# Kernel optimization log

Hardware: AMD Instinct MI355X
Metric: run time of the kernel (lower is better)

Reference implementation:

```python
import jax, jax.numpy as jnp
import numpy as np

N_NODES = 100000
N_EDGES = 3200000
F_IN = 64
HID = 20
N_GRAPHS = 128
N_CLASSES = 10
EPS_NORM = 1e-12  # torch F.normalize eps


def setup_inputs() -> dict:
    key = jax.random.key(0)
    ks = jax.random.split(key, 16)
    x = jax.random.normal(ks[0], (N_NODES, F_IN), dtype=jnp.float32)
    edge_index = jax.random.randint(ks[1], (2, N_EDGES), 0, N_NODES, dtype=jnp.int64)
    batch = jnp.sort(jax.random.randint(ks[2], (N_NODES,), 0, N_GRAPHS, dtype=jnp.int64))
    edge_weights = jnp.ones((N_EDGES,), dtype=jnp.float32)

    def lin_init(k, fan_in, fan_out):
        kw, kb = jax.random.split(k)
        bound = 1.0 / np.sqrt(fan_in)
        W = jax.random.uniform(kw, (fan_in, fan_out), jnp.float32, -bound, bound)
        b = jax.random.uniform(kb, (fan_out,), jnp.float32, -bound, bound)
        return W, b

    W1a, b1a = lin_init(ks[3], F_IN, HID)
    W1b, b1b = lin_init(ks[4], HID, HID)
    W2a, b2a = lin_init(ks[5], HID, HID)
    W2b, b2b = lin_init(ks[6], HID, HID)
    W3a, b3a = lin_init(ks[7], HID, HID)
    W3b, b3b = lin_init(ks[8], HID, HID)
    Wlin, blin = lin_init(ks[9], 2 * HID, N_CLASSES)
    return dict(x=x, edge_index=edge_index, batch=batch, edge_weights=edge_weights,
                W1a=W1a, b1a=b1a, W1b=W1b, b1b=b1b,
                W2a=W2a, b2a=b2a, W2b=W2b, b2b=b2b,
                W3a=W3a, b3a=b3a, W3b=W3b, b3b=b3b,
                Wlin=Wlin, blin=blin)


def _gin_layer(h, src, dst, w, Wa, ba, Wb, bb):
    # scatter-add aggregation: agg[dst] += h[src] * w   (no self-loop / central term
    # because edge_weight is provided in GINConv_mask.forward)
    msg = h[src] * w[:, None]                              # [E, d]
    agg = jax.ops.segment_sum(msg, dst, num_segments=N_NODES)
    z = jax.nn.relu(agg @ Wa + ba)
    z = jax.nn.relu(z @ Wb + bb)
    # per-node L2 normalize then ReLU
    nrm = jnp.sqrt(jnp.sum(z * z, axis=1, keepdims=True))
    z = z / jnp.maximum(nrm, EPS_NORM)
    return jax.nn.relu(z)


def reference(x, edge_index, batch, edge_weights,
              W1a, b1a, W1b, b1b, W2a, b2a, W2b, b2b, W3a, b3a, W3b, b3b,
              Wlin, blin):
    src, dst = edge_index[0], edge_index[1]
    h = _gin_layer(x, src, dst, edge_weights, W1a, b1a, W1b, b1b)
    h = _gin_layer(h, src, dst, edge_weights, W2a, b2a, W2b, b2b)
    h = _gin_layer(h, src, dst, edge_weights, W3a, b3a, W3b, b3b)  # [N, 20]

    # global max / mean pool per graph
    mx = jax.ops.segment_max(h, batch, num_segments=N_GRAPHS)
    counts = jax.ops.segment_sum(jnp.ones((N_NODES,), h.dtype), batch, num_segments=N_GRAPHS)
    sm = jax.ops.segment_sum(h, batch, num_segments=N_GRAPHS)
    mean = sm / jnp.maximum(counts, 1.0)[:, None]
    mx = jnp.where(counts[:, None] > 0, mx, 0.0)
    pooled = jnp.concatenate([mx, mean], axis=-1)          # [G, 40]
    return pooled @ Wlin + blin                            # [G, num_classes]
```

## Files before the change

### kernel.cpp

```cpp
#include <hip/hip_runtime.h>
#include <hip/hip_fp16.h>
#include <math.h>

#define NN 100000
#define NE 3200000
#define FIN 64
#define HID 20
#define NG 128
#define NC 10

#define BSH 8
#define NB1 391
#define NB1P 392
#define NBLK1 1024
#define E1 (NE / NBLK1)

__global__ __launch_bounds__(256) void k_in_gemm_h(const float* __restrict__ x,
                                                   const float* __restrict__ W,
                                                   __half* __restrict__ t) {
    __shared__ float sW[FIN * HID];
    for (int i = threadIdx.x; i < FIN * HID; i += blockDim.x) sW[i] = W[i];
    __syncthreads();
    int node = blockIdx.x * blockDim.x + threadIdx.x;
    if (node >= NN) return;
    float acc[HID];
#pragma unroll
    for (int f = 0; f < HID; ++f) acc[f] = 0.f;
    const float4* xr = (const float4*)(x + node * FIN);
#pragma unroll 4
    for (int q = 0; q < FIN / 4; ++q) {
        float4 xv = xr[q];
        int k = q * 4;
#pragma unroll
        for (int f = 0; f < HID; ++f) acc[f] += xv.x * sW[(k + 0) * HID + f];
#pragma unroll
        for (int f = 0; f < HID; ++f) acc[f] += xv.y * sW[(k + 1) * HID + f];
#pragma unroll
        for (int f = 0; f < HID; ++f) acc[f] += xv.z * sW[(k + 2) * HID + f];
#pragma unroll
        for (int f = 0; f < HID; ++f) acc[f] += xv.w * sW[(k + 3) * HID + f];
    }
    uint32_t* orow = (uint32_t*)t + (size_t)node * (HID / 2);
#pragma unroll
    for (int m = 0; m < HID / 2; ++m) {
        __half2 hh = __floats2half2_rn(acc[2 * m], acc[2 * m + 1]);
        orow[m] = *reinterpret_cast<uint32_t*>(&hh);
    }
}

__global__ __launch_bounds__(256) void k_p1count(const int* __restrict__ dst,
                                                 int* __restrict__ ghist) {
    __shared__ int h[NB1];
    for (int i = threadIdx.x; i < NB1; i += 256) h[i] = 0;
    __syncthreads();
    int base = blockIdx.x * E1;
    for (int i = threadIdx.x; i < E1; i += 256)
        atomicAdd(&h[dst[base + i] >> BSH], 1);
    __syncthreads();
    for (int b = threadIdx.x; b < NB1; b += 256)
        ghist[b * NBLK1 + blockIdx.x] = h[b];
}

__global__ __launch_bounds__(256) void k_breduceB(const int* __restrict__ ghist,
                                                  int* __restrict__ bsum) {
    int bin = blockIdx.x;
    int s = 0;
    for (int i = threadIdx.x; i < NBLK1; i += 256) s += ghist[bin * NBLK1 + i];
    __shared__ int r[256];
    r[threadIdx.x] = s;
    __syncthreads();
    for (int o = 128; o > 0; o >>= 1) {
        if (threadIdx.x < o) r[threadIdx.x] += r[threadIdx.x + o];
        __syncthreads();
    }
    if (threadIdx.x == 0) bsum[bin] = r[0];
}

__global__ __launch_bounds__(256) void k_bscanB(const int* __restrict__ bsum,
                                                int* __restrict__ bstart) {
    __shared__ int s[NB1];
    for (int i = threadIdx.x; i < NB1; i += 256) s[i] = bsum[i];
    __syncthreads();
    if (threadIdx.x == 0) {
        int acc = 0;
        for (int i = 0; i < NB1; ++i) { int v = s[i]; s[i] = acc; acc += v; }
    }
    __syncthreads();
    for (int i = threadIdx.x; i < NB1; i += 256) bstart[i] = s[i];
    if (threadIdx.x == 0) bstart[NB1] = NE;
}

__global__ __launch_bounds__(256) void k_bbase(const int* __restrict__ ghist,
                                               const int* __restrict__ bstart,
                                               int* __restrict__ gbase) {
    int bin = blockIdx.x;
    int t = threadIdx.x;
    int v[4];
    int s = 0;
    int base = bin * NBLK1 + t * 4;
#pragma unroll
    for (int k = 0; k < 4; ++k) { v[k] = ghist[base + k]; s += v[k]; }
    __shared__ int tsum[256];
    tsum[t] = s;
    __syncthreads();
    for (int d = 1; d < 256; d <<= 1) {
        int add = (t >= d) ? tsum[t - d] : 0;
        __syncthreads();
        tsum[t] += add;
        __syncthreads();
    }
    int excl = tsum[t] - s + bstart[bin];
#pragma unroll
    for (int k = 0; k < 4; ++k) {
        gbase[(size_t)(t * 4 + k) * NB1P + bin] = excl;
        excl += v[k];
    }
}

__global__ __launch_bounds__(256) void k_p1scatter(const int* __restrict__ src,
                                                   const int* __restrict__ dst,
                                                   const float* __restrict__ w,
                                                   const int* __restrict__ gbase,
                                                   int2* __restrict__ part) {
    __shared__ int cur[NB1];
    int t = threadIdx.x;
    for (int b = t; b < NB1; b += 256) cur[b] = gbase[(size_t)blockIdx.x * NB1P + b];
    __syncthreads();
    int base = blockIdx.x * E1;
    for (int i = t; i < E1; i += 256) {
        int e = base + i;
        int d = dst[e];
        int b = d >> BSH;
        int pos = atomicAdd(&cur[b], 1);
        part[pos] = make_int2(src[e] | ((d & 255) << 17), __float_as_int(w[e]));
    }
}

__global__ __launch_bounds__(256) void k_p2(const int2* __restrict__ part,
                                            const int* __restrict__ bstart,
                                            int2* __restrict__ csr,
                                            int* __restrict__ off) {
    int b = blockIdx.x;
    int lo = bstart[b], hi = bstart[b + 1];
    int t = threadIdx.x;
    __shared__ int hist[256];
    hist[t] = 0;
    __syncthreads();
    for (int i = lo + t; i < hi; i += 256)
        atomicAdd(&hist[part[i].x >> 17], 1);
    __syncthreads();
    int a = hist[t];
    __shared__ int tsum[256];
    tsum[t] = a;
    __syncthreads();
    for (int d = 1; d < 256; d <<= 1) {
        int add = (t >= d) ? tsum[t - d] : 0;
        __syncthreads();
        tsum[t] += add;
        __syncthreads();
    }
    int excl = tsum[t] - a;
    __shared__ int cur[256];
    cur[t] = lo + excl;
    int node = (b << BSH) + t;
    if (node < NN) off[node] = lo + excl;
    if (b == NB1 - 1 && t == 0) off[NN] = NE;
    __syncthreads();
    for (int i = lo + t; i < hi; i += 256) {
        int2 pr = part[i];
        int ld = pr.x >> 17;
        int pos = atomicAdd(&cur[ld], 1);
        csr[pos] = make_int2(pr.x & 0x1FFFF, pr.y);
    }
}

template <bool LAST>
__global__ __launch_bounds__(256) void k_layer(const int* __restrict__ off,
                                               const int2* __restrict__ csr,
                                               const __half* __restrict__ tin,
                                               const float* __restrict__ ba,
                                               const float* __restrict__ Wb,
                                               const float* __restrict__ bb,
                                               const float* __restrict__ Wnext,
                                               __half* __restrict__ tout) {
    __shared__ float sWb[HID * HID];
    __shared__ float sWn[HID * HID];
    __shared__ float sba[HID], sbb[HID];
    for (int i = threadIdx.x; i < HID * HID; i += blockDim.x) {
        sWb[i] = Wb[i];
        if (!LAST) sWn[i] = Wnext[i];
    }
    if (threadIdx.x < HID) {
        sba[threadIdx.x] = ba[threadIdx.x];
        sbb[threadIdx.x] = bb[threadIdx.x];
    }
    __syncthreads();

    int tid = blockIdx.x * blockDim.x + threadIdx.x;
    int node = tid >> 2;
    int j = tid & 3;
    if (node >= NN) return;
    int lo = off[node], hi = off[node + 1];

    float acc[HID];
#pragma unroll
    for (int f = 0; f < HID; ++f) acc[f] = 0.f;

    for (int i = lo + j; i < hi; i += 4) {
        int2 pr = csr[i];
        float wt = __int_as_float(pr.y);
        const uint2* r = (const uint2*)tin + (size_t)pr.x * 5;
#pragma unroll
        for (int k = 0; k < 5; ++k) {
            uint2 u = r[k];
            __half2 h0 = *reinterpret_cast<const __half2*>(&u.x);
            __half2 h1 = *reinterpret_cast<const __half2*>(&u.y);
            float2 f0 = __half22float2(h0);
            float2 f1 = __half22float2(h1);
            acc[4 * k + 0] += wt * f0.x;
            acc[4 * k + 1] += wt * f0.y;
            acc[4 * k + 2] += wt * f1.x;
            acc[4 * k + 3] += wt * f1.y;
        }
    }
#pragma unroll
    for (int f = 0; f < HID; ++f) {
        acc[f] += __shfl_xor(acc[f], 1);
        acc[f] += __shfl_xor(acc[f], 2);
    }

    float z1[HID];
#pragma unroll
    for (int f = 0; f < HID; ++f) z1[f] = fmaxf(acc[f] + sba[f], 0.f);

    float z2[HID];
#pragma unroll
    for (int fo = 0; fo < HID; ++fo) {
        float a = sbb[fo];
#pragma unroll
        for (int k = 0; k < HID; ++k) a += z1[k] * sWb[k * HID + fo];
        z2[fo] = fmaxf(a, 0.f);
    }

    float ss = 0.f;
#pragma unroll
    for (int f = 0; f < HID; ++f) ss += z2[f] * z2[f];
    float scale = 1.f / fmaxf(sqrtf(ss), 1e-12f);
#pragma unroll
    for (int f = 0; f < HID; ++f) z2[f] *= scale;

    float res[HID];
    if (LAST) {
#pragma unroll
        for (int f = 0; f < HID; ++f) res[f] = z2[f];
    } else {
#pragma unroll
        for (int fo = 0; fo < HID; ++fo) {
            float a = 0.f;
#pragma unroll
            for (int k = 0; k < HID; ++k) a += z2[k] * sWn[k * HID + fo];
            res[fo] = a;
        }
    }

    uint32_t* orow = (uint32_t*)tout + (size_t)node * (HID / 2);
#pragma unroll
    for (int m0 = 0; m0 < 12; m0 += 4) {
        int m = m0 + j;
        if (m < HID / 2) {
            __half2 hh = __floats2half2_rn(res[2 * m], res[2 * m + 1]);
            orow[m] = *reinterpret_cast<uint32_t*>(&hh);
        }
    }
}

__global__ __launch_bounds__(256) void k_pool_h(const __half* __restrict__ h,
                                                const int* __restrict__ batch,
                                                const float* __restrict__ Wlin,
                                                const float* __restrict__ blin,
                                                float* __restrict__ out) {
    int g = blockIdx.x;
    __shared__ int s_lo, s_hi;
    if (threadIdx.x == 0) {
        int a = 0, b = NN;
        while (a < b) { int m = (a + b) >> 1; if (batch[m] < g) a = m + 1; else b = m; }
        s_lo = a;
        b = NN;
        while (a < b) { int m = (a + b) >> 1; if (batch[m] < g + 1) a = m + 1; else b = m; }
        s_hi = a;
    }
    __syncthreads();
    int lo = s_lo, hi = s_hi;

    float sm[HID], mx[HID];
#pragma unroll
    for (int f = 0; f < HID; ++f) { sm[f] = 0.f; mx[f] = 0.f; }

    for (int i = lo + threadIdx.x; i < hi; i += blockDim.x) {
        const uint2* hr = (const uint2*)h + (size_t)i * 5;
#pragma unroll
        for (int k = 0; k < 5; ++k) {
            uint2 u = hr[k];
            __half2 h0 = *reinterpret_cast<const __half2*>(&u.x);
            __half2 h1 = *reinterpret_cast<const __half2*>(&u.y);
            float2 f0 = __half22float2(h0);
            float2 f1 = __half22float2(h1);
            sm[4 * k + 0] += f0.x; mx[4 * k + 0] = fmaxf(mx[4 * k + 0], f0.x);
            sm[4 * k + 1] += f0.y; mx[4 * k + 1] = fmaxf(mx[4 * k + 1], f0.y);
            sm[4 * k + 2] += f1.x; mx[4 * k + 2] = fmaxf(mx[4 * k + 2], f1.x);
            sm[4 * k + 3] += f1.y; mx[4 * k + 3] = fmaxf(mx[4 * k + 3], f1.y);
        }
    }

#pragma unroll
    for (int f = 0; f < HID; ++f) {
        float s = sm[f], m = mx[f];
        for (int off = 32; off > 0; off >>= 1) {
            s += __shfl_down(s, off);
            m = fmaxf(m, __shfl_down(m, off));
        }
        sm[f] = s; mx[f] = m;
    }

    __shared__ float psum[4][HID], pmax[4][HID];
    int wave = threadIdx.x >> 6;
    int lane = threadIdx.x & 63;
    if (lane == 0) {
#pragma unroll
        for (int f = 0; f < HID; ++f) { psum[wave][f] = sm[f]; pmax[wave][f] = mx[f]; }
    }
    __syncthreads();

    __shared__ float fsum[HID], fmax_[HID];
    if (threadIdx.x < HID) {
        int f = threadIdx.x;
        fsum[f] = psum[0][f] + psum[1][f] + psum[2][f] + psum[3][f];
        fmax_[f] = fmaxf(fmaxf(pmax[0][f], pmax[1][f]), fmaxf(pmax[2][f], pmax[3][f]));
    }
    __syncthreads();

    if (threadIdx.x < NC) {
        int c = threadIdx.x;
        float cnt = (float)(hi - lo);
        float inv = 1.f / fmaxf(cnt, 1.f);
        float o = blin[c];
#pragma unroll
        for (int f = 0; f < HID; ++f) {
            o += fmax_[f] * Wlin[f * NC + c];
            o += (fsum[f] * inv) * Wlin[(HID + f) * NC + c];
        }
        out[g * NC + c] = o;
    }
}

__global__ __launch_bounds__(256) void k_in_gemm(const float* __restrict__ x,
                                                 const float* __restrict__ W,
                                                 float* __restrict__ t) {
    __shared__ float sW[FIN * HID];
    for (int i = threadIdx.x; i < FIN * HID; i += blockDim.x) sW[i] = W[i];
    __syncthreads();
    int node = blockIdx.x * blockDim.x + threadIdx.x;
    if (node >= NN) return;
    float acc[HID];
#pragma unroll
    for (int f = 0; f < HID; ++f) acc[f] = 0.f;
    const float4* xr = (const float4*)(x + node * FIN);
    for (int q = 0; q < FIN / 4; ++q) {
        float4 xv = xr[q];
        int k = q * 4;
#pragma unroll
        for (int f = 0; f < HID; ++f)
            acc[f] += xv.x * sW[k * HID + f] + xv.y * sW[(k + 1) * HID + f] +
                      xv.z * sW[(k + 2) * HID + f] + xv.w * sW[(k + 3) * HID + f];
    }
    float4* tr = (float4*)(t + node * HID);
#pragma unroll
    for (int q = 0; q < HID / 4; ++q) {
        float4 v;
        v.x = acc[q * 4 + 0]; v.y = acc[q * 4 + 1];
        v.z = acc[q * 4 + 2]; v.w = acc[q * 4 + 3];
        tr[q] = v;
    }
}

__global__ __launch_bounds__(256) void k_scatter(const int* __restrict__ src,
                                                 const int* __restrict__ dst,
                                                 const float* __restrict__ w,
                                                 const float* __restrict__ t,
                                                 float* __restrict__ agg) {
    int e = blockIdx.x * blockDim.x + threadIdx.x;
    if (e >= NE) return;
    int s = src[e];
    int d = dst[e];
    float wt = w[e];
    const float4* tr = (const float4*)(t + (long)s * HID);
    float* ar = agg + (long)d * HID;
#pragma unroll
    for (int q = 0; q < HID / 4; ++q) {
        float4 v = tr[q];
        atomicAdd(ar + q * 4 + 0, v.x * wt);
        atomicAdd(ar + q * 4 + 1, v.y * wt);
        atomicAdd(ar + q * 4 + 2, v.z * wt);
        atomicAdd(ar + q * 4 + 3, v.w * wt);
    }
}

template <bool LAST>
__global__ __launch_bounds__(256) void k_node(const float* agg,
                                              const float* __restrict__ ba,
                                              const float* __restrict__ Wb,
                                              const float* __restrict__ bb,
                                              const float* __restrict__ Wnext,
                                              float* out) {
    __shared__ float sWb[HID * HID];
    __shared__ float sWn[HID * HID];
    __shared__ float sba[HID], sbb[HID];
    for (int i = threadIdx.x; i < HID * HID; i += blockDim.x) {
        sWb[i] = Wb[i];
        if (!LAST) sWn[i] = Wnext[i];
    }
    if (threadIdx.x < HID) {
        sba[threadIdx.x] = ba[threadIdx.x];
        sbb[threadIdx.x] = bb[threadIdx.x];
    }
    __syncthreads();
    int node = blockIdx.x * blockDim.x + threadIdx.x;
    if (node >= NN) return;

    float z1[HID];
    const float4* ar = (const float4*)(agg + (long)node * HID);
#pragma unroll
    for (int q = 0; q < HID / 4; ++q) {
        float4 v = ar[q];
        z1[q * 4 + 0] = v.x; z1[q * 4 + 1] = v.y;
        z1[q * 4 + 2] = v.z; z1[q * 4 + 3] = v.w;
    }
#pragma unroll
    for (int f = 0; f < HID; ++f) z1[f] = fmaxf(z1[f] + sba[f], 0.f);

    float z2[HID];
#pragma unroll
    for (int fo = 0; fo < HID; ++fo) {
        float a = sbb[fo];
#pragma unroll
        for (int k = 0; k < HID; ++k) a += z1[k] * sWb[k * HID + fo];
        z2[fo] = fmaxf(a, 0.f);
    }
    float ss = 0.f;
#pragma unroll
    for (int f = 0; f < HID; ++f) ss += z2[f] * z2[f];
    float scale = 1.f / fmaxf(sqrtf(ss), 1e-12f);
#pragma unroll
    for (int f = 0; f < HID; ++f) z2[f] *= scale;

    float res[HID];
    if (LAST) {
#pragma unroll
        for (int f = 0; f < HID; ++f) res[f] = z2[f];
    } else {
#pragma unroll
        for (int fo = 0; fo < HID; ++fo) {
            float a = 0.f;
#pragma unroll
            for (int k = 0; k < HID; ++k) a += z2[k] * sWn[k * HID + fo];
            res[fo] = a;
        }
    }
    float4* orow = (float4*)(out + (long)node * HID);
#pragma unroll
    for (int q = 0; q < HID / 4; ++q) {
        float4 v;
        v.x = res[q * 4 + 0]; v.y = res[q * 4 + 1];
        v.z = res[q * 4 + 2]; v.w = res[q * 4 + 3];
        orow[q] = v;
    }
}

__global__ __launch_bounds__(256) void k_pool(const float* __restrict__ h,
                                              const int* __restrict__ batch,
                                              const float* __restrict__ Wlin,
                                              const float* __restrict__ blin,
                                              float* __restrict__ out) {
    int g = blockIdx.x;
    __shared__ int s_lo, s_hi;
    if (threadIdx.x == 0) {
        int a = 0, b = NN;
        while (a < b) { int m = (a + b) >> 1; if (batch[m] < g) a = m + 1; else b = m; }
        s_lo = a;
        b = NN;
        while (a < b) { int m = (a + b) >> 1; if (batch[m] < g + 1) a = m + 1; else b = m; }
        s_hi = a;
    }
    __syncthreads();
    int lo = s_lo, hi = s_hi;
    float sm[HID], mx[HID];
#pragma unroll
    for (int f = 0; f < HID; ++f) { sm[f] = 0.f; mx[f] = 0.f; }
    for (int i = lo + threadIdx.x; i < hi; i += blockDim.x) {
        const float4* hr = (const float4*)(h + (long)i * HID);
#pragma unroll
        for (int q = 0; q < HID / 4; ++q) {
            float4 v = hr[q];
            sm[q * 4 + 0] += v.x; mx[q * 4 + 0] = fmaxf(mx[q * 4 + 0], v.x);
            sm[q * 4 + 1] += v.y; mx[q * 4 + 1] = fmaxf(mx[q * 4 + 1], v.y);
            sm[q * 4 + 2] += v.z; mx[q * 4 + 2] = fmaxf(mx[q * 4 + 2], v.z);
            sm[q * 4 + 3] += v.w; mx[q * 4 + 3] = fmaxf(mx[q * 4 + 3], v.w);
        }
    }
#pragma unroll
    for (int f = 0; f < HID; ++f) {
        float s = sm[f], m = mx[f];
        for (int off = 32; off > 0; off >>= 1) {
            s += __shfl_down(s, off);
            m = fmaxf(m, __shfl_down(m, off));
        }
        sm[f] = s; mx[f] = m;
    }
    __shared__ float psum[4][HID], pmax[4][HID];
    int wave = threadIdx.x >> 6;
    int lane = threadIdx.x & 63;
    if (lane == 0) {
#pragma unroll
        for (int f = 0; f < HID; ++f) { psum[wave][f] = sm[f]; pmax[wave][f] = mx[f]; }
    }
    __syncthreads();
    __shared__ float fsum[HID], fmax_[HID];
    if (threadIdx.x < HID) {
        int f = threadIdx.x;
        fsum[f] = psum[0][f] + psum[1][f] + psum[2][f] + psum[3][f];
        fmax_[f] = fmaxf(fmaxf(pmax[0][f], pmax[1][f]), fmaxf(pmax[2][f], pmax[3][f]));
    }
    __syncthreads();
    if (threadIdx.x < NC) {
        int c = threadIdx.x;
        float cnt = (float)(hi - lo);
        float inv = 1.f / fmaxf(cnt, 1.f);
        float o = blin[c];
#pragma unroll
        for (int f = 0; f < HID; ++f) {
            o += fmax_[f] * Wlin[f * NC + c];
            o += (fsum[f] * inv) * Wlin[(HID + f) * NC + c];
        }
        out[g * NC + c] = o;
    }
}

extern "C" void kernel_launch(void* const* d_in, const int* in_sizes, int n_in,
                              void* d_out, int out_size, void* d_ws, size_t ws_size,
                              hipStream_t stream) {
    const float* x   = (const float*)d_in[0];
    const int*   ei  = (const int*)d_in[1];
    const int*   bat = (const int*)d_in[2];
    const float* ew  = (const float*)d_in[3];
    const float* W1a = (const float*)d_in[4];
    const float* b1a = (const float*)d_in[5];
    const float* W1b = (const float*)d_in[6];
    const float* b1b = (const float*)d_in[7];
    const float* W2a = (const float*)d_in[8];
    const float* b2a = (const float*)d_in[9];
    const float* W2b = (const float*)d_in[10];
    const float* b2b = (const float*)d_in[11];
    const float* W3a = (const float*)d_in[12];
    const float* b3a = (const float*)d_in[13];
    const float* W3b = (const float*)d_in[14];
    const float* b3b = (const float*)d_in[15];
    const float* Wlin = (const float*)d_in[16];
    const float* blin = (const float*)d_in[17];

    const int* src = ei;
    const int* dst = ei + NE;

    dim3 blk(256);
    dim3 gN((NN + 255) / 256);
    dim3 gE((NE + 255) / 256);
    dim3 gQ(((size_t)NN * 4 + 255) / 256);

    size_t szT    = (size_t)NN * HID * sizeof(float);
    size_t szCsr  = (size_t)NE * sizeof(int2);
    size_t szOff  = ((size_t)(NN + 1) * sizeof(int) + 15) & ~(size_t)15;
    size_t szGh   = (size_t)NB1 * NBLK1 * sizeof(int);
    size_t szGb   = (size_t)NBLK1 * NB1P * sizeof(int);
    size_t szSm   = 2048;
    size_t szTh   = (size_t)NN * HID * sizeof(__half);
    size_t szPart = szCsr > 2 * szTh ? szCsr : 2 * szTh;
    size_t need_radix = szCsr + szOff + szGh + szGb + 2 * szSm + szPart;

    if (ws_size >= need_radix) {
        char* p = (char*)d_ws;
        int2* csr    = (int2*)p;  p += szCsr;
        int*  offv   = (int*)p;   p += szOff;
        int*  ghist  = (int*)p;   p += szGh;
        int*  gbase  = (int*)p;   p += szGb;
        int*  bsum   = (int*)p;   p += szSm;
        int*  bstart = (int*)p;   p += szSm;
        int2* part   = (int2*)p;
        __half* T0h = (__half*)part;
        __half* T1h = T0h + (size_t)NN * HID;

        k_p1count<<<NBLK1, blk, 0, stream>>>(dst, ghist);
        k_breduceB<<<NB1, blk, 0, stream>>>(ghist, bsum);
        k_bscanB<<<1, blk, 0, stream>>>(bsum, bstart);
        k_bbase<<<NB1, blk, 0, stream>>>(ghist, bstart, gbase);
        k_p1scatter<<<NBLK1, blk, 0, stream>>>(src, dst, ew, gbase, part);
        k_p2<<<NB1, blk, 0, stream>>>(part, bstart, csr, offv);

        k_in_gemm_h<<<gN, blk, 0, stream>>>(x, W1a, T0h);
        k_layer<false><<<gQ, blk, 0, stream>>>(offv, csr, T0h, b1a, W1b, b1b, W2a, T1h);
        k_layer<false><<<gQ, blk, 0, stream>>>(offv, csr, T1h, b2a, W2b, b2b, W3a, T0h);
        k_layer<true><<<gQ, blk, 0, stream>>>(offv, csr, T0h, b3a, W3b, b3b, nullptr, T1h);

        k_pool_h<<<NG, blk, 0, stream>>>(T1h, bat, Wlin, blin, (float*)d_out);
    } else {
        char* p = (char*)d_ws;
        float* T0 = (float*)p;  p += szT;
        float* T1 = (float*)p;

        k_in_gemm<<<gN, blk, 0, stream>>>(x, W1a, T0);
        hipMemsetAsync(T1, 0, szT, stream);
        k_scatter<<<gE, blk, 0, stream>>>(src, dst, ew, T0, T1);
        k_node<false><<<gN, blk, 0, stream>>>(T1, b1a, W1b, b1b, W2a, T0);
        hipMemsetAsync(T1, 0, szT, stream);
        k_scatter<<<gE, blk, 0, stream>>>(src, dst, ew, T0, T1);
        k_node<false><<<gN, blk, 0, stream>>>(T1, b2a, W2b, b2b, W3a, T0);
        hipMemsetAsync(T1, 0, szT, stream);
        k_scatter<<<gE, blk, 0, stream>>>(src, dst, ew, T0, T1);
        k_node<true><<<gN, blk, 0, stream>>>(T1, b3a, W3b, b3b, nullptr, T0);
        k_pool<<<NG, blk, 0, stream>>>(T0, bat, Wlin, blin, (float*)d_out);
    }
}
```

Baseline: 304.7 us.

## Use 8 lanes per node with dual accumulators, XCD block swizzle, nontemporal CSR loads

The GIN layer kernel now assigns 8 threads per node instead of 4, with each thread handling two edges per iteration into separate accumulators and an extra shuffle stage in the reduction. This raises memory-level parallelism on the feature-row gathers. The partition kernels remap block IDs so contiguous edge chunks are grouped per XCD, and the CSR/partition streams are read with nontemporal loads to avoid polluting cache. In exchange the kernel uses more registers and launches twice as many threads.

```diff
diff --git a/kernel.cpp b/kernel.cpp
--- a/kernel.cpp
+++ b/kernel.cpp
@@ -14,6 +14,11 @@
 #define NB1P 392
 #define NBLK1 1024
 #define E1 (NE / NBLK1)
+#define NXCD 8
+
+__device__ __forceinline__ int swz_blk(int bid) {
+    return (bid & (NXCD - 1)) * (NBLK1 / NXCD) + (bid >> 3);
+}
 
 __global__ __launch_bounds__(256) void k_in_gemm_h(const float* __restrict__ x,
                                                    const float* __restrict__ W,
@@ -53,12 +58,13 @@
     __shared__ int h[NB1];
     for (int i = threadIdx.x; i < NB1; i += 256) h[i] = 0;
     __syncthreads();
-    int base = blockIdx.x * E1;
+    int lb = swz_blk(blockIdx.x);
+    int base = lb * E1;
     for (int i = threadIdx.x; i < E1; i += 256)
         atomicAdd(&h[dst[base + i] >> BSH], 1);
     __syncthreads();
     for (int b = threadIdx.x; b < NB1; b += 256)
-        ghist[b * NBLK1 + blockIdx.x] = h[b];
+        ghist[b * NBLK1 + lb] = h[b];
 }
 
 __global__ __launch_bounds__(256) void k_breduceB(const int* __restrict__ ghist,
@@ -124,9 +130,10 @@
                                                    int2* __restrict__ part) {
     __shared__ int cur[NB1];
     int t = threadIdx.x;
-    for (int b = t; b < NB1; b += 256) cur[b] = gbase[(size_t)blockIdx.x * NB1P + b];
-    __syncthreads();
-    int base = blockIdx.x * E1;
+    int lb = swz_blk(blockIdx.x);
+    for (int b = t; b < NB1; b += 256) cur[b] = gbase[(size_t)lb * NB1P + b];
+    __syncthreads();
+    int base = lb * E1;
     for (int i = t; i < E1; i += 256) {
         int e = base + i;
         int d = dst[e];
@@ -146,8 +153,10 @@
     __shared__ int hist[256];
     hist[t] = 0;
     __syncthreads();
-    for (int i = lo + t; i < hi; i += 256)
-        atomicAdd(&hist[part[i].x >> 17], 1);
+    for (int i = lo + t; i < hi; i += 256) {
+        int v = __builtin_nontemporal_load(&part[i].x);
+        atomicAdd(&hist[v >> 17], 1);
+    }
     __syncthreads();
     int a = hist[t];
     __shared__ int tsum[256];
@@ -166,11 +175,30 @@
     if (node < NN) off[node] = lo + excl;
     if (b == NB1 - 1 && t == 0) off[NN] = NE;
     __syncthreads();
+    const long long* pp = (const long long*)part;
     for (int i = lo + t; i < hi; i += 256) {
-        int2 pr = part[i];
-        int ld = pr.x >> 17;
+        long long pv = __builtin_nontemporal_load(pp + i);
+        int px = (int)pv;
+        int ld = px >> 17;
         int pos = atomicAdd(&cur[ld], 1);
-        csr[pos] = make_int2(pr.x & 0x1FFFF, pr.y);
+        csr[pos] = make_int2(px & 0x1FFFF, (int)(pv >> 32));
+    }
+}
+
+__device__ __forceinline__ void gather_row(const __half* __restrict__ tin,
+                                           int srcn, float wt, float* acc) {
+    const uint2* r = (const uint2*)tin + (size_t)srcn * 5;
+#pragma unroll
+    for (int k = 0; k < 5; ++k) {
+        uint2 u = r[k];
+        __half2 h0 = *reinterpret_cast<const __half2*>(&u.x);
+        __half2 h1 = *reinterpret_cast<const __half2*>(&u.y);
+        float2 f0 = __half22float2(h0);
+        float2 f1 = __half22float2(h1);
+        acc[4 * k + 0] += wt * f0.x;
+        acc[4 * k + 1] += wt * f0.y;
+        acc[4 * k + 2] += wt * f1.x;
+        acc[4 * k + 3] += wt * f1.y;
     }
 }
 
@@ -197,41 +225,39 @@
     __syncthreads();
 
     int tid = blockIdx.x * blockDim.x + threadIdx.x;
-    int node = tid >> 2;
-    int j = tid & 3;
+    int node = tid >> 3;
+    int j = tid & 7;
     if (node >= NN) return;
     int lo = off[node], hi = off[node + 1];
 
-    float acc[HID];
-#pragma unroll
-    for (int f = 0; f < HID; ++f) acc[f] = 0.f;
-
-    for (int i = lo + j; i < hi; i += 4) {
-        int2 pr = csr[i];
-        float wt = __int_as_float(pr.y);
-        const uint2* r = (const uint2*)tin + (size_t)pr.x * 5;
-#pragma unroll
-        for (int k = 0; k < 5; ++k) {
-            uint2 u = r[k];
-            __half2 h0 = *reinterpret_cast<const __half2*>(&u.x);
-            __half2 h1 = *reinterpret_cast<const __half2*>(&u.y);
-            float2 f0 = __half22float2(h0);
-            float2 f1 = __half22float2(h1);
-            acc[4 * k + 0] += wt * f0.x;
-            acc[4 * k + 1] += wt * f0.y;
-            acc[4 * k + 2] += wt * f1.x;
-            acc[4 * k + 3] += wt * f1.y;
+    float a0[HID], a1[HID];
+#pragma unroll
+    for (int f = 0; f < HID; ++f) { a0[f] = 0.f; a1[f] = 0.f; }
+
+    const long long* pc = (const long long*)csr;
+    for (int i = lo + j; i < hi; i += 16) {
+        long long v0 = __builtin_nontemporal_load(pc + i);
+        int px0 = (int)v0;
+        gather_row(tin, px0 & 0x1FFFF, __int_as_float((int)(v0 >> 32)), a0);
+        int i2 = i + 8;
+        if (i2 < hi) {
+            long long v1 = __builtin_nontemporal_load(pc + i2);
+            int px1 = (int)v1;
+            gather_row(tin, px1 & 0x1FFFF, __int_as_float((int)(v1 >> 32)), a1);
         }
     }
 #pragma unroll
     for (int f = 0; f < HID; ++f) {
-        acc[f] += __shfl_xor(acc[f], 1);
-        acc[f] += __shfl_xor(acc[f], 2);
+        float a = a0[f] + a1[f];
+        a += __shfl_xor(a, 1);
+        a += __shfl_xor(a, 2);
+        a += __shfl_xor(a, 4);
+        a0[f] = a;
     }
 
     float z1[HID];
 #pragma unroll
-    for (int f = 0; f < HID; ++f) z1[f] = fmaxf(acc[f] + sba[f], 0.f);
+    for (int f = 0; f < HID; ++f) z1[f] = fmaxf(a0[f] + sba[f], 0.f);
 
     float z2[HID];
 #pragma unroll
@@ -265,7 +291,7 @@
 
     uint32_t* orow = (uint32_t*)tout + (size_t)node * (HID / 2);
 #pragma unroll
-    for (int m0 = 0; m0 < 12; m0 += 4) {
+    for (int m0 = 0; m0 < 16; m0 += 8) {
         int m = m0 + j;
         if (m < HID / 2) {
             __half2 hh = __floats2half2_rn(res[2 * m], res[2 * m + 1]);
@@ -570,10 +596,8 @@
     const int* src = ei;
     const int* dst = ei + NE;
 
-    dim3 blk(256);
     dim3 gN((NN + 255) / 256);
-    dim3 gE((NE + 255) / 256);
-    dim3 gQ(((size_t)NN * 4 + 255) / 256);
+    dim3 gQ8(((size_t)NN * 8 + 255) / 256);
 
     size_t szT    = (size_t)NN * HID * sizeof(float);
     size_t szCsr  = (size_t)NE * sizeof(int2);
@@ -597,34 +621,35 @@
         __half* T0h = (__half*)part;
         __half* T1h = T0h + (size_t)NN * HID;
 
-        k_p1count<<<NBLK1, blk, 0, stream>>>(dst, ghist);
-        k_breduceB<<<NB1, blk, 0, stream>>>(ghist, bsum);
-        k_bscanB<<<1, blk, 0, stream>>>(bsum, bstart);
-        k_bbase<<<NB1, blk, 0, stream>>>(ghist, bstart, gbase);
-        k_p1scatter<<<NBLK1, blk, 0, stream>>>(src, dst, ew, gbase, part);
-        k_p2<<<NB1, blk, 0, stream>>>(part, bstart, csr, offv);
-
-        k_in_gemm_h<<<gN, blk, 0, stream>>>(x, W1a, T0h);
-        k_layer<false><<<gQ, blk, 0, stream>>>(offv, csr, T0h, b1a, W1b, b1b, W2a, T1h);
-        k_layer<false><<<gQ, blk, 0, stream>>>(offv, csr, T1h, b2a, W2b, b2b, W3a, T0h);
-        k_layer<true><<<gQ, blk, 0, stream>>>(offv, csr, T0h, b3a, W3b, b3b, nullptr, T1h);
-
-        k_pool_h<<<NG, blk, 0, stream>>>(T1h, bat, Wlin, blin, (float*)d_out);
+        k_p1count<<<NBLK1, 256, 0, stream>>>(dst, ghist);
+        k_breduceB<<<NB1, 256, 0, stream>>>(ghist, bsum);
+        k_bscanB<<<1, 256, 0, stream>>>(bsum, bstart);
+        k_bbase<<<NB1, 256, 0, stream>>>(ghist, bstart, gbase);
+        k_p1scatter<<<NBLK1, 256, 0, stream>>>(src, dst, ew, gbase, part);
+        k_p2<<<NB1, 256, 0, stream>>>(part, bstart, csr, offv);
+
+        k_in_gemm_h<<<gN, 256, 0, stream>>>(x, W1a, T0h);
+        k_layer<false><<<gQ8, 256, 0, stream>>>(offv, csr, T0h, b1a, W1b, b1b, W2a, T1h);
+        k_layer<false><<<gQ8, 256, 0, stream>>>(offv, csr, T1h, b2a, W2b, b2b, W3a, T0h);
+        k_layer<true><<<gQ8, 256, 0, stream>>>(offv, csr, T0h, b3a, W3b, b3b, nullptr, T1h);
+
+        k_pool_h<<<NG, 256, 0, stream>>>(T1h, bat, Wlin, blin, (float*)d_out);
     } else {
         char* p = (char*)d_ws;
         float* T0 = (float*)p;  p += szT;
         float* T1 = (float*)p;
-
-        k_in_gemm<<<gN, blk, 0, stream>>>(x, W1a, T0);
+        dim3 gE((NE + 255) / 256);
+
+        k_in_gemm<<<gN, 256, 0, stream>>>(x, W1a, T0);
         hipMemsetAsync(T1, 0, szT, stream);
-        k_scatter<<<gE, blk, 0, stream>>>(src, dst, ew, T0, T1);
-        k_node<false><<<gN, blk, 0, stream>>>(T1, b1a, W1b, b1b, W2a, T0);
+        k_scatter<<<gE, 256, 0, stream>>>(src, dst, ew, T0, T1);
+        k_node<false><<<gN, 256, 0, stream>>>(T1, b1a, W1b, b1b, W2a, T0);
         hipMemsetAsync(T1, 0, szT, stream);
-        k_scatter<<<gE, blk, 0, stream>>>(src, dst, ew, T0, T1);
-        k_node<false><<<gN, blk, 0, stream>>>(T1, b2a, W2b, b2b, W3a, T0);
+        k_scatter<<<gE, 256, 0, stream>>>(src, dst, ew, T0, T1);
+        k_node<false><<<gN, 256, 0, stream>>>(T1, b2a, W2b, b2b, W3a, T0);
         hipMemsetAsync(T1, 0, szT, stream);
-        k_scatter<<<gE, blk, 0, stream>>>(src, dst, ew, T0, T1);
-        k_node<true><<<gN, blk, 0, stream>>>(T1, b3a, W3b, b3b, nullptr, T0);
-        k_pool<<<NG, blk, 0, stream>>>(T0, bat, Wlin, blin, (float*)d_out);
-    }
-}
+        k_scatter<<<gE, 256, 0, stream>>>(src, dst, ew, T0, T1);
+        k_node<true><<<gN, 256, 0, stream>>>(T1, b3a, W3b, b3b, nullptr, T0);
+        k_pool<<<NG, 256, 0, stream>>>(T0, bat, Wlin, blin, (float*)d_out);
+    }
+}
```

Result: slower. 332.6 us (+9.1%).
